# Optimization experiments

Hardware: AMD Instinct MI355X
Metric: run time of the kernel (lower is better)

Reference implementation:

```python
import jax, jax.numpy as jnp
import numpy as np

N = 50000      # nodes per graph type
E = 600000     # directed edges
F = 64         # raw node feature length
H = 128        # hidden / embedding size (embedding == h, so no padding needed)
STEPS = 4
G = 64         # graphs in batch


def setup_inputs() -> dict:
    key = jax.random.key(0)
    ks = jax.random.split(key, 16)
    s = 1.0 / np.sqrt(H)
    inp = {
        "atom_x": jax.random.normal(ks[0], (N, F), jnp.float32),
        "voro_x": jax.random.normal(ks[1], (N, F), jnp.float32),
        "atom_edge_index": jax.random.randint(ks[2], (2, E), 0, N, jnp.int64),
        "voro_edge_index": jax.random.randint(ks[3], (2, E), 0, N, jnp.int64),
        "batch": jnp.sort(jax.random.randint(ks[4], (N,), 0, G, jnp.int64)),
        # input embeddings (bias=False)
        "W_atom_in": jax.random.normal(ks[5], (F, H), jnp.float32) / np.sqrt(F),
        "W_voro_in": jax.random.normal(ks[6], (F, H), jnp.float32) / np.sqrt(F),
        # GatedGraphConv per-step message weights [STEPS, H, H]
        "atom_W": jax.random.normal(ks[7], (STEPS, H, H), jnp.float32) * s,
        "voro_W": jax.random.normal(ks[8], (STEPS, H, H), jnp.float32) * s,
        # GRUCell params (torch layout: W_ih [3H, H], gates ordered r, z, n)
        "atom_Wih": jax.random.normal(ks[9], (3 * H, H), jnp.float32) * s,
        "atom_Whh": jax.random.normal(ks[10], (3 * H, H), jnp.float32) * s,
        "atom_bih": jnp.zeros((3 * H,), jnp.float32),
        "atom_bhh": jnp.zeros((3 * H,), jnp.float32),
        "voro_Wih": jax.random.normal(ks[11], (3 * H, H), jnp.float32) * s,
        "voro_Whh": jax.random.normal(ks[12], (3 * H, H), jnp.float32) * s,
        "voro_bih": jnp.zeros((3 * H,), jnp.float32),
        "voro_bhh": jnp.zeros((3 * H,), jnp.float32),
        # prediction head Linear(2H, 1)
        "pred_W": jax.random.normal(ks[13], (2 * H, 1), jnp.float32) * s,
        "pred_b": jnp.zeros((1,), jnp.float32),
    }
    return inp


def _gated_graph_conv(x, edge_index, W, Wih, Whh, bih, bhh):
    """PyG GatedGraphConv with aggr='add': per step, m = h @ W_l, scatter-add
    messages from source to target, then GRUCell(m, h)."""
    src, dst = edge_index[0], edge_index[1]

    def step(h, Wl):
        m = h @ Wl                                           # [N, H]
        agg = jax.ops.segment_sum(m[src], dst, num_segments=N)  # gather+scatter-add
        gi = agg @ Wih.T + bih                               # input gates
        gh = h @ Whh.T + bhh                                 # hidden gates
        ir, iz, inn = jnp.split(gi, 3, axis=-1)
        hr, hz, hn = jnp.split(gh, 3, axis=-1)
        r = jax.nn.sigmoid(ir + hr)
        z = jax.nn.sigmoid(iz + hz)
        n = jnp.tanh(inn + r * hn)
        h_new = (1.0 - z) * n + z * h
        return h_new, None

    h, _ = jax.lax.scan(step, x, W)
    return h


def _mean_pool(x, batch):
    s = jax.ops.segment_sum(x, batch, num_segments=G)
    cnt = jax.ops.segment_sum(jnp.ones((x.shape[0],), x.dtype), batch, num_segments=G)
    return s / jnp.maximum(cnt, 1.0)[:, None]


def reference(atom_x, voro_x, atom_edge_index, voro_edge_index, batch,
              W_atom_in, W_voro_in, atom_W, voro_W,
              atom_Wih, atom_Whh, atom_bih, atom_bhh,
              voro_Wih, voro_Whh, voro_bih, voro_bhh,
              pred_W, pred_b):
    a = jnp.tanh(atom_x @ W_atom_in)                         # [N, H]
    v = jnp.tanh(voro_x @ W_voro_in)                         # [N, H]
    a = _gated_graph_conv(a, atom_edge_index, atom_W, atom_Wih, atom_Whh, atom_bih, atom_bhh)
    v = _gated_graph_conv(v, voro_edge_index, voro_W, voro_Wih, voro_Whh, voro_bih, voro_bhh)
    a = jax.nn.relu(_mean_pool(a, batch))                    # [G, H]
    v = jax.nn.relu(_mean_pool(v, batch))                    # [G, H]
    g = jnp.concatenate([a, v], axis=1)                      # [G, 2H]
    return (g @ pred_W + pred_b)[:, 0]                       # [G]
```

## Files before the change

kernel.cpp:

```cpp
#include <hip/hip_runtime.h>
#include <hip/hip_fp16.h>
#include <math.h>

#define HDIM 128
typedef unsigned short u16;
typedef __attribute__((ext_vector_type(8))) short bf16x8;
typedef __attribute__((ext_vector_type(4))) float f32x4;

__device__ __forceinline__ u16 f2bf(float x) {
    unsigned u = __float_as_uint(x);
    u = (u + 0x7FFFu + ((u >> 16) & 1u)) >> 16;
    return (u16)u;
}
__device__ __forceinline__ float bf2f(u16 h) {
    return __uint_as_float(((unsigned)h) << 16);
}
__device__ __forceinline__ bf16x8 ld8(const u16* p) {
    return *reinterpret_cast<const bf16x8*>(p);
}
__device__ __forceinline__ void split8(const float* v, bf16x8& hi, bf16x8& lo) {
#pragma unroll
    for (int j = 0; j < 8; ++j) {
        unsigned u = __float_as_uint(v[j]);
        unsigned h = (u + 0x7FFFu + ((u >> 16) & 1u)) >> 16;
        float rem = v[j] - __uint_as_float(h << 16);
        hi[j] = (short)h;
        lo[j] = (short)(__float_as_uint(rem) >> 16);
    }
}
__device__ __forceinline__ float2 up2(unsigned u) {
    __half2 h = *reinterpret_cast<__half2*>(&u);
    float2 f; f.x = __low2float(h); f.y = __high2float(h); return f;
}
__device__ __forceinline__ u16 f2h(float x) {
    __half t = __float2half(x);
    return *reinterpret_cast<u16*>(&t);
}
#define MFMA(acc, a, b) acc = __builtin_amdgcn_mfma_f32_16x16x32_bf16(a, b, acc, 0, 0, 0)

__global__ __launch_bounds__(256) void prep_wfull(const float* __restrict__ Ws,
                                                  const float* __restrict__ Wih,
                                                  u16* __restrict__ hi, u16* __restrict__ lo) {
    int s = blockIdx.y;
    int idx = blockIdx.x * 256 + threadIdx.x;
    int c2 = idx >> 7, r = idx & 127;
    const float* wr = Ws + (size_t)s * 16384 + (size_t)r * 128;
    const float* wc = Wih + (size_t)c2 * 128;
    float acc = 0.f;
#pragma unroll 8
    for (int k = 0; k < 128; k += 4) {
        float4 a = *reinterpret_cast<const float4*>(wr + k);
        float4 b = *reinterpret_cast<const float4*>(wc + k);
        acc += a.x * b.x + a.y * b.y + a.z * b.z + a.w * b.w;
    }
    size_t o = (size_t)s * 49152 + idx;
    u16 h = f2bf(acc);
    hi[o] = h; lo[o] = f2bf(acc - bf2f(h));
}

__global__ __launch_bounds__(256) void prep_split(const float* __restrict__ W,
                                                  u16* __restrict__ hi, u16* __restrict__ lo, int n) {
    int i = blockIdx.x * 256 + threadIdx.x;
    if (i < n) { float v = W[i]; u16 h = f2bf(v); hi[i] = h; lo[i] = f2bf(v - bf2f(h)); }
}

__global__ __launch_bounds__(256) void prep_win(const float* __restrict__ W,
                                                u16* __restrict__ hi, u16* __restrict__ lo) {
    int idx = blockIdx.x * 256 + threadIdx.x;
    int r = idx >> 6, c = idx & 63;
    float v = W[(size_t)c * 128 + r];
    u16 h = f2bf(v);
    hi[idx] = h; lo[idx] = f2bf(v - bf2f(h));
}

__global__ __launch_bounds__(256) void split_x2(const float* __restrict__ x0, const float* __restrict__ x1,
                                                u16* __restrict__ hi0, u16* __restrict__ lo0,
                                                u16* __restrict__ hi1, u16* __restrict__ lo1,
                                                int n, int ntot) {
    int i = blockIdx.x * 256 + threadIdx.x;
    if (i >= ntot) return;
    const float* x = blockIdx.y ? x1 : x0;
    u16* hi = blockIdx.y ? hi1 : hi0;
    u16* lo = blockIdx.y ? lo1 : lo0;
    float v = (i < n) ? x[i] : 0.f;
    u16 h = f2bf(v);
    hi[i] = h; lo[i] = f2bf(v - bf2f(h));
}

__global__ __launch_bounds__(256) void embed_k(const u16* __restrict__ Xhi0, const u16* __restrict__ Xlo0,
                                               const u16* __restrict__ Xhi1, const u16* __restrict__ Xlo1,
                                               const u16* __restrict__ Bhi0, const u16* __restrict__ Blo0,
                                               const u16* __restrict__ Bhi1, const u16* __restrict__ Blo1,
                                               float* __restrict__ Hf0, float* __restrict__ Hf1,
                                               u16* __restrict__ Hh0, u16* __restrict__ Hh1) {
    const int by = blockIdx.y;
    const u16* Xhi = by ? Xhi1 : Xhi0;  const u16* Xlo = by ? Xlo1 : Xlo0;
    const u16* Bhi = by ? Bhi1 : Bhi0;  const u16* Blo = by ? Blo1 : Blo0;
    float* Hf = by ? Hf1 : Hf0;
    u16* Hh = by ? Hh1 : Hh0;
    const int tid = threadIdx.x, wave = tid >> 6, lane = tid & 63;
    const int row0 = blockIdx.x * 32, cs = wave * 32;
    const int lr = lane & 15, lk = (lane >> 4) * 8;
    f32x4 acc[2][2];
#pragma unroll
    for (int i = 0; i < 2; ++i)
#pragma unroll
        for (int j = 0; j < 2; ++j) acc[i][j] = (f32x4)0.f;
#pragma unroll
    for (int kc = 0; kc < 2; ++kc) {
        const size_t ao = (size_t)(row0 + lr) * 64 + kc * 32 + lk;
        bf16x8 ah0 = ld8(Xhi + ao), ah1 = ld8(Xhi + ao + 16 * 64);
        bf16x8 al0 = ld8(Xlo + ao), al1 = ld8(Xlo + ao + 16 * 64);
#pragma unroll
        for (int cf = 0; cf < 2; ++cf) {
            const size_t bo = (size_t)(cs + cf * 16 + lr) * 64 + kc * 32 + lk;
            bf16x8 bh = ld8(Bhi + bo), bl = ld8(Blo + bo);
            MFMA(acc[0][cf], ah0, bh); MFMA(acc[0][cf], ah0, bl); MFMA(acc[0][cf], al0, bh);
            MFMA(acc[1][cf], ah1, bh); MFMA(acc[1][cf], ah1, bl); MFMA(acc[1][cf], al1, bh);
        }
    }
#pragma unroll
    for (int rf = 0; rf < 2; ++rf)
#pragma unroll
        for (int cf = 0; cf < 2; ++cf)
#pragma unroll
            for (int rg = 0; rg < 4; ++rg) {
                int row = row0 + rf * 16 + (lane >> 4) * 4 + rg;
                int col = cs + cf * 16 + lr;
                float v = tanhf(acc[rf][cf][rg]);
                size_t o = (size_t)row * HDIM + col;
                Hf[o] = v;
                Hh[o] = f2h(v);
            }
}

__global__ __launch_bounds__(512, 4) void step_k(const float* __restrict__ Hf0, const float* __restrict__ Hf1,
                                                 const u16* __restrict__ Hh0, const u16* __restrict__ Hh1,
                                                 const int* __restrict__ ro0, const int* __restrict__ ro1,
                                                 const int* __restrict__ ss0, const int* __restrict__ ss1,
                                                 const u16* __restrict__ Wf0h, const u16* __restrict__ Wf0l,
                                                 const u16* __restrict__ Wf1h, const u16* __restrict__ Wf1l,
                                                 const u16* __restrict__ Wh0h, const u16* __restrict__ Wh0l,
                                                 const u16* __restrict__ Wh1h, const u16* __restrict__ Wh1l,
                                                 const float* __restrict__ bi0, const float* __restrict__ bh0,
                                                 const float* __restrict__ bi1, const float* __restrict__ bh1,
                                                 float* __restrict__ Hn0, float* __restrict__ Hn1,
                                                 u16* __restrict__ Hnh0, u16* __restrict__ Hnh1, int Nn) {
    __shared__ u16 agh[32][136];
    __shared__ u16 agl[32][136];
    __shared__ u16 hhh[32][136];
    __shared__ u16 hhl[32][136];
    __shared__ int eidx[1024];
    const int by = blockIdx.y;
    const float* Hf = by ? Hf1 : Hf0;
    const u16* Hh = by ? Hh1 : Hh0;
    const int* row_off = by ? ro1 : ro0;
    const int* ssrc = by ? ss1 : ss0;
    const int tid = threadIdx.x, wave = tid >> 6, lane = tid & 63;
    const int row0 = blockIdx.x * 32;

    const int rowEnd = (row0 + 32 < Nn) ? row0 + 32 : Nn;
    const int eLo = row_off[row0];
    const int nE = row_off[rowEnd] - eLo;
    for (int i = tid; i < nE && i < 1024; i += 512) eidx[i] = ssrc[eLo + i];
    __syncthreads();

#pragma unroll
    for (int q = 0; q < 4; ++q) {
        const int nl = wave * 4 + q;
        const int node = row0 + nl;
        float ax = 0.f, ay = 0.f;
        if (node < Nn) {
            int lo = row_off[node] - eLo, hi = row_off[node + 1] - eLo;
            int hiS = (hi < 1024) ? hi : 1024;
            int i = lo;
            for (; i + 12 <= hiS; i += 12) {
                unsigned u[12];
#pragma unroll
                for (int j = 0; j < 12; ++j)
                    u[j] = *reinterpret_cast<const unsigned*>(Hh + (size_t)eidx[i + j] * HDIM + lane * 2);
#pragma unroll
                for (int j = 0; j < 12; ++j) { float2 v = up2(u[j]); ax += v.x; ay += v.y; }
            }
            for (; i + 4 <= hiS; i += 4) {
                unsigned u[4];
#pragma unroll
                for (int j = 0; j < 4; ++j)
                    u[j] = *reinterpret_cast<const unsigned*>(Hh + (size_t)eidx[i + j] * HDIM + lane * 2);
#pragma unroll
                for (int j = 0; j < 4; ++j) { float2 v = up2(u[j]); ax += v.x; ay += v.y; }
            }
            for (; i < hiS; ++i) {
                float2 v = up2(*reinterpret_cast<const unsigned*>(Hh + (size_t)eidx[i] * HDIM + lane * 2));
                ax += v.x; ay += v.y;
            }
            for (; i < hi; ++i) {
                float2 v = up2(*reinterpret_cast<const unsigned*>(Hh + (size_t)ssrc[eLo + i] * HDIM + lane * 2));
                ax += v.x; ay += v.y;
            }
        }
        u16 hx = f2bf(ax), hy = f2bf(ay);
        u16 lx = f2bf(ax - bf2f(hx)), ly = f2bf(ay - bf2f(hy));
        *reinterpret_cast<unsigned*>(&agh[nl][lane * 2]) = (unsigned)hx | ((unsigned)hy << 16);
        *reinterpret_cast<unsigned*>(&agl[nl][lane * 2]) = (unsigned)lx | ((unsigned)ly << 16);
    }

    {
        const int r = tid >> 4, c0 = (tid & 15) * 8;
        float v[8];
        const float* hp = Hf + (size_t)(row0 + r) * HDIM + c0;
        *reinterpret_cast<float4*>(&v[0]) = *reinterpret_cast<const float4*>(hp);
        *reinterpret_cast<float4*>(&v[4]) = *reinterpret_cast<const float4*>(hp + 4);
        bf16x8 hi, lo;
        split8(v, hi, lo);
        *reinterpret_cast<bf16x8*>(&hhh[r][c0]) = hi;
        *reinterpret_cast<bf16x8*>(&hhl[r][c0]) = lo;
    }
    __syncthreads();

    const u16* Wfhi = by ? Wf1h : Wf0h;  const u16* Wflo = by ? Wf1l : Wf0l;
    const u16* Whhi = by ? Wh1h : Wh0h;  const u16* Whlo = by ? Wh1l : Wh0l;
    const float* bih = by ? bi1 : bi0;   const float* bhh = by ? bh1 : bh0;
    float* Hnf = by ? Hn1 : Hn0;
    u16* Hnh = by ? Hnh1 : Hnh0;
    const int lr = lane & 15, lk = (lane >> 4) * 8, cs = wave * 16;
    f32x4 accI[2][3], accH[2][3];
#pragma unroll
    for (int rf = 0; rf < 2; ++rf)
#pragma unroll
        for (int g = 0; g < 3; ++g) { accI[rf][g] = (f32x4)0.f; accH[rf][g] = (f32x4)0.f; }
#pragma unroll
    for (int kc = 0; kc < 4; ++kc) {
        bf16x8 ga[2], gl[2], ha[2], hl[2];
#pragma unroll
        for (int rf = 0; rf < 2; ++rf) {
            const int rr = rf * 16 + lr, cc = kc * 32 + lk;
            ga[rf] = *reinterpret_cast<const bf16x8*>(&agh[rr][cc]);
            gl[rf] = *reinterpret_cast<const bf16x8*>(&agl[rr][cc]);
            ha[rf] = *reinterpret_cast<const bf16x8*>(&hhh[rr][cc]);
            hl[rf] = *reinterpret_cast<const bf16x8*>(&hhl[rr][cc]);
        }
#pragma unroll
        for (int g = 0; g < 3; ++g) {
            const size_t bo = (size_t)(g * 128 + cs + lr) * HDIM + kc * 32 + lk;
            bf16x8 fh = ld8(Wfhi + bo), fl = ld8(Wflo + bo);
            bf16x8 wh = ld8(Whhi + bo), wl = ld8(Whlo + bo);
#pragma unroll
            for (int rf = 0; rf < 2; ++rf) {
                MFMA(accI[rf][g], ga[rf], fh); MFMA(accI[rf][g], ga[rf], fl); MFMA(accI[rf][g], gl[rf], fh);
                MFMA(accH[rf][g], ha[rf], wh); MFMA(accH[rf][g], ha[rf], wl); MFMA(accH[rf][g], hl[rf], wh);
            }
        }
    }
    const int c = cs + lr;
    const float bir = bih[c], biz = bih[128 + c], bin = bih[256 + c];
    const float bhr = bhh[c], bhz = bhh[128 + c], bhn = bhh[256 + c];
#pragma unroll
    for (int rf = 0; rf < 2; ++rf)
#pragma unroll
        for (int rg = 0; rg < 4; ++rg) {
            const int rl = rf * 16 + (lane >> 4) * 4 + rg;
            const int row = row0 + rl;
            float gir = accI[rf][0][rg] + bir;
            float giz = accI[rf][1][rg] + biz;
            float gin = accI[rf][2][rg] + bin;
            float ghr = accH[rf][0][rg] + bhr;
            float ghz = accH[rf][1][rg] + bhz;
            float ghn = accH[rf][2][rg] + bhn;
            float r = 1.f / (1.f + expf(-(gir + ghr)));
            float z = 1.f / (1.f + expf(-(giz + ghz)));
            float nn = tanhf(gin + r * ghn);
            float hold = bf2f(hhh[rl][c]) + bf2f(hhl[rl][c]);
            float hn = (1.f - z) * nn + z * hold;
            size_t o = (size_t)row * HDIM + c;
            Hnf[o] = hn;
            Hnh[o] = f2h(hn);
        }
}

__global__ void zero_int2(int* p0, int* p1, int n) {
    int i = blockIdx.x * 256 + threadIdx.x;
    int* p = blockIdx.y ? p1 : p0;
    if (i < n) p[i] = 0;
}

__global__ void hist_k2(const int* __restrict__ d0, const int* __restrict__ d1,
                        int* __restrict__ c0, int* __restrict__ c1, int E) {
    int e = blockIdx.x * 256 + threadIdx.x;
    const int* dst = blockIdx.y ? d1 : d0;
    int* cnt = blockIdx.y ? c1 : c0;
    if (e < E) atomicAdd(&cnt[dst[e]], 1);
}

__global__ __launch_bounds__(1024) void scan_k2(int* __restrict__ c0, int* __restrict__ r0,
                                                int* __restrict__ c1, int* __restrict__ r1, int n) {
    int* cnt_cursor = blockIdx.x ? c1 : c0;
    int* row_off = blockIdx.x ? r1 : r0;
    __shared__ int wsum[16];
    __shared__ int carry_s;
    const int tid = threadIdx.x, lane = tid & 63, wv = tid >> 6;
    if (tid == 0) carry_s = 0;
    __syncthreads();
    for (int base = 0; base < n; base += 1024) {
        int i = base + tid;
        int v = (i < n) ? cnt_cursor[i] : 0;
        int x = v;
#pragma unroll
        for (int off = 1; off < 64; off <<= 1) {
            int t = __shfl_up(x, off);
            if (lane >= off) x += t;
        }
        if (lane == 63) wsum[wv] = x;
        __syncthreads();
        if (wv == 0 && lane < 16) {
            int s = wsum[lane];
#pragma unroll
            for (int off = 1; off < 16; off <<= 1) {
                int t = __shfl_up(s, off);
                if (lane >= off) s += t;
            }
            wsum[lane] = s;
        }
        __syncthreads();
        int wbase = (wv == 0) ? 0 : wsum[wv - 1];
        int carry = carry_s;
        int total = wsum[15];
        int excl = carry + wbase + x - v;
        if (i < n) { row_off[i] = excl; cnt_cursor[i] = excl; }
        __syncthreads();
        if (tid == 0) carry_s = carry + total;
        __syncthreads();
    }
    if (tid == 0) row_off[n] = carry_s;
}

__global__ void scatter_k2(const int* __restrict__ s0, const int* __restrict__ d0,
                           const int* __restrict__ s1, const int* __restrict__ d1,
                           int* __restrict__ c0, int* __restrict__ c1,
                           int* __restrict__ o0, int* __restrict__ o1, int E) {
    int e = blockIdx.x * 256 + threadIdx.x;
    const int* src = blockIdx.y ? s1 : s0;
    const int* dst = blockIdx.y ? d1 : d0;
    int* cursor = blockIdx.y ? c1 : c0;
    int* ssrc = blockIdx.y ? o1 : o0;
    if (e < E) {
        int p = atomicAdd(&cursor[dst[e]], 1);
        ssrc[p] = src[e];
    }
}

__global__ __launch_bounds__(256) void pool_k(const float* __restrict__ H0, const float* __restrict__ H1,
                                              const int* __restrict__ batch,
                                              float* __restrict__ p0, float* __restrict__ p1, int M) {
    const float* Hf = blockIdx.y ? H1 : H0;
    float* pooled = blockIdx.y ? p1 : p0;
    __shared__ int lo_s, hi_s;
    __shared__ float smx[256], smy[256];
    int g = blockIdx.x;
    if (threadIdx.x == 0) {
        int lo = 0, hi = M;
        while (lo < hi) { int mid = (lo + hi) >> 1; if (batch[mid] < g) lo = mid + 1; else hi = mid; }
        lo_s = lo;
        int lo2 = lo, hi2 = M;
        while (lo2 < hi2) { int mid = (lo2 + hi2) >> 1; if (batch[mid] < g + 1) lo2 = mid + 1; else hi2 = mid; }
        hi_s = lo2;
    }
    __syncthreads();
    int lo = lo_s, hi = hi_s;
    int c2 = threadIdx.x & 63, quarter = threadIdx.x >> 6;
    float ax = 0.f, ay = 0.f;
    for (int i = lo + quarter; i < hi; i += 4) {
        float2 v = *reinterpret_cast<const float2*>(Hf + (size_t)i * HDIM + c2 * 2);
        ax += v.x; ay += v.y;
    }
    smx[threadIdx.x] = ax; smy[threadIdx.x] = ay;
    __syncthreads();
    if (quarter == 0) {
        float sx = smx[c2] + smx[c2 + 64] + smx[c2 + 128] + smx[c2 + 192];
        float sy = smy[c2] + smy[c2 + 64] + smy[c2 + 128] + smy[c2 + 192];
        float cnt = (float)(hi - lo); if (cnt < 1.f) cnt = 1.f;
        pooled[g * HDIM + c2 * 2]     = fmaxf(sx / cnt, 0.f);
        pooled[g * HDIM + c2 * 2 + 1] = fmaxf(sy / cnt, 0.f);
    }
}

__global__ void pred_kernel(const float* __restrict__ pa, const float* __restrict__ pv,
                            const float* __restrict__ pW, const float* __restrict__ pb,
                            float* __restrict__ out) {
    int g = blockIdx.x, lane = threadIdx.x;
    float s = pa[g * HDIM + lane] * pW[lane]
            + pa[g * HDIM + 64 + lane] * pW[64 + lane]
            + pv[g * HDIM + lane] * pW[HDIM + lane]
            + pv[g * HDIM + 64 + lane] * pW[192 + lane];
    for (int off = 32; off; off >>= 1) s += __shfl_down(s, off);
    if (lane == 0) out[g] = s + pb[0];
}

extern "C" void kernel_launch(void* const* d_in, const int* in_sizes, int n_in,
                              void* d_out, int out_size, void* d_ws, size_t ws_size,
                              hipStream_t stream) {
    const float* atom_x   = (const float*)d_in[0];
    const float* voro_x   = (const float*)d_in[1];
    const int*   atom_ei  = (const int*)d_in[2];
    const int*   voro_ei  = (const int*)d_in[3];
    const int*   batch    = (const int*)d_in[4];
    const float* W_at_in  = (const float*)d_in[5];
    const float* W_vo_in  = (const float*)d_in[6];
    const float* atom_W   = (const float*)d_in[7];
    const float* voro_W   = (const float*)d_in[8];
    const float* atom_Wih = (const float*)d_in[9];
    const float* atom_Whh = (const float*)d_in[10];
    const float* atom_bih = (const float*)d_in[11];
    const float* atom_bhh = (const float*)d_in[12];
    const float* voro_Wih = (const float*)d_in[13];
    const float* voro_Whh = (const float*)d_in[14];
    const float* voro_bih = (const float*)d_in[15];
    const float* voro_bhh = (const float*)d_in[16];
    const float* pred_W   = (const float*)d_in[17];
    const float* pred_b   = (const float*)d_in[18];
    float* out = (float*)d_out;

    const int Nn = in_sizes[4];
    const int Ee = in_sizes[2] / 2;
    const int Gg = out_size;
    const int Npad = (Nn + 31) & ~31;

    char* base = (char*)d_ws;
    size_t off = 0;
    auto alloc = [&](size_t bytes) -> char* {
        char* p = base + off;
        off = (off + bytes + 255) & ~(size_t)255;
        return p;
    };

    float *Hf[2], *Hnf[2];
    u16 *HhA[2], *HhB[2];
    u16 *Xhi[2], *Xlo[2];
    u16 *WfHi[2], *WfLo[2], *WhHi[2], *WhLo[2], *WnHi[2], *WnLo[2];
    int *row_off[2], *cursor[2], *ssrc[2];
    for (int t = 0; t < 2; ++t) {
        Hf[t]  = (float*)alloc((size_t)Npad * HDIM * 4);
        Hnf[t] = (float*)alloc((size_t)Npad * HDIM * 4);
        HhA[t] = (u16*)alloc((size_t)Npad * HDIM * 2);
        HhB[t] = (u16*)alloc((size_t)Npad * HDIM * 2);
        Xhi[t] = (u16*)Hnf[t];
        Xlo[t] = Xhi[t] + (size_t)Npad * 64;
        WfHi[t] = (u16*)alloc(4 * 49152 * 2); WfLo[t] = (u16*)alloc(4 * 49152 * 2);
        WhHi[t] = (u16*)alloc(384 * 128 * 2); WhLo[t] = (u16*)alloc(384 * 128 * 2);
        WnHi[t] = (u16*)alloc(128 * 64 * 2);  WnLo[t] = (u16*)alloc(128 * 64 * 2);
        row_off[t] = (int*)alloc((size_t)(Nn + 1) * 4);
        cursor[t]  = (int*)alloc((size_t)Nn * 4);
        ssrc[t]    = (int*)alloc((size_t)Ee * 4);
    }
    float* pooledA = (float*)alloc((size_t)Gg * HDIM * 4);
    float* pooledV = (float*)alloc((size_t)Gg * HDIM * 4);

    const float* Wst[2] = {atom_W, voro_W};
    const float* Wih[2] = {atom_Wih, voro_Wih};
    const float* Whh[2] = {atom_Whh, voro_Whh};
    const float* Win[2] = {W_at_in, W_vo_in};

    for (int t = 0; t < 2; ++t) {
        prep_wfull<<<dim3(192, 4), 256, 0, stream>>>(Wst[t], Wih[t], WfHi[t], WfLo[t]);
        prep_split<<<192, 256, 0, stream>>>(Whh[t], WhHi[t], WhLo[t], 384 * 128);
        prep_win<<<32, 256, 0, stream>>>(Win[t], WnHi[t], WnLo[t]);
    }

    const int eb  = (Ee + 255) / 256;
    const int nb  = (Nn + 255) / 256;
    const int gbs = Npad / 32;

    split_x2<<<dim3((Npad * 64 + 255) / 256, 2), 256, 0, stream>>>(
        atom_x, voro_x, Xhi[0], Xlo[0], Xhi[1], Xlo[1], Nn * 64, Npad * 64);
    embed_k<<<dim3(gbs, 2), 256, 0, stream>>>(Xhi[0], Xlo[0], Xhi[1], Xlo[1],
                                              WnHi[0], WnLo[0], WnHi[1], WnLo[1],
                                              Hf[0], Hf[1], HhA[0], HhA[1]);

    zero_int2<<<dim3(nb, 2), 256, 0, stream>>>(cursor[0], cursor[1], Nn);
    hist_k2<<<dim3(eb, 2), 256, 0, stream>>>(atom_ei + Ee, voro_ei + Ee, cursor[0], cursor[1], Ee);
    scan_k2<<<2, 1024, 0, stream>>>(cursor[0], row_off[0], cursor[1], row_off[1], Nn);
    scatter_k2<<<dim3(eb, 2), 256, 0, stream>>>(atom_ei, atom_ei + Ee, voro_ei, voro_ei + Ee,
                                                cursor[0], cursor[1], ssrc[0], ssrc[1], Ee);

    float *hA0 = Hf[0], *hB0 = Hnf[0], *hA1 = Hf[1], *hB1 = Hnf[1];
    u16 *gA0 = HhA[0], *gB0 = HhB[0], *gA1 = HhA[1], *gB1 = HhB[1];
    for (int s = 0; s < 4; ++s) {
        step_k<<<dim3(gbs, 2), 512, 0, stream>>>(
            hA0, hA1, gA0, gA1, row_off[0], row_off[1], ssrc[0], ssrc[1],
            WfHi[0] + (size_t)s * 49152, WfLo[0] + (size_t)s * 49152,
            WfHi[1] + (size_t)s * 49152, WfLo[1] + (size_t)s * 49152,
            WhHi[0], WhLo[0], WhHi[1], WhLo[1],
            atom_bih, atom_bhh, voro_bih, voro_bhh,
            hB0, hB1, gB0, gB1, Nn);
        float* tp;
        tp = hA0; hA0 = hB0; hB0 = tp;
        tp = hA1; hA1 = hB1; hB1 = tp;
        u16* up;
        up = gA0; gA0 = gB0; gB0 = up;
        up = gA1; gA1 = gB1; gB1 = up;
    }
    pool_k<<<dim3(Gg, 2), 256, 0, stream>>>(hA0, hA1, batch, pooledA, pooledV, Nn);
    pred_kernel<<<Gg, 64, 0, stream>>>(pooledA, pooledV, pred_W, pred_b, out);
}
```

Baseline: 1.166 ms.

## Drop fp32 hidden-state copy and interleave gathers across four nodes per wave

Removes the fp32 copy of the hidden state. Embedding, step and pooling kernels now read and write only the 16-bit copy, which cuts global traffic and workspace, and the input split buffers alias the spare 16-bit buffer. The neighbour aggregation now handles a wave's four nodes together, issuing 16 masked gathers per iteration up to the largest degree to raise memory-level parallelism. The cost is lower precision on the carried hidden state and wasted loads when degrees are imbalanced.

```diff
diff --git a/kernel.cpp b/kernel.cpp
--- a/kernel.cpp
+++ b/kernel.cpp
@@ -91,12 +91,10 @@
                                                const u16* __restrict__ Xhi1, const u16* __restrict__ Xlo1,
                                                const u16* __restrict__ Bhi0, const u16* __restrict__ Blo0,
                                                const u16* __restrict__ Bhi1, const u16* __restrict__ Blo1,
-                                               float* __restrict__ Hf0, float* __restrict__ Hf1,
                                                u16* __restrict__ Hh0, u16* __restrict__ Hh1) {
     const int by = blockIdx.y;
     const u16* Xhi = by ? Xhi1 : Xhi0;  const u16* Xlo = by ? Xlo1 : Xlo0;
     const u16* Bhi = by ? Bhi1 : Bhi0;  const u16* Blo = by ? Blo1 : Blo0;
-    float* Hf = by ? Hf1 : Hf0;
     u16* Hh = by ? Hh1 : Hh0;
     const int tid = threadIdx.x, wave = tid >> 6, lane = tid & 63;
     const int row0 = blockIdx.x * 32, cs = wave * 32;
@@ -127,15 +125,11 @@
             for (int rg = 0; rg < 4; ++rg) {
                 int row = row0 + rf * 16 + (lane >> 4) * 4 + rg;
                 int col = cs + cf * 16 + lr;
-                float v = tanhf(acc[rf][cf][rg]);
-                size_t o = (size_t)row * HDIM + col;
-                Hf[o] = v;
-                Hh[o] = f2h(v);
+                Hh[(size_t)row * HDIM + col] = f2h(tanhf(acc[rf][cf][rg]));
             }
 }
 
-__global__ __launch_bounds__(512, 4) void step_k(const float* __restrict__ Hf0, const float* __restrict__ Hf1,
-                                                 const u16* __restrict__ Hh0, const u16* __restrict__ Hh1,
+__global__ __launch_bounds__(512, 4) void step_k(const u16* __restrict__ Hh0, const u16* __restrict__ Hh1,
                                                  const int* __restrict__ ro0, const int* __restrict__ ro1,
                                                  const int* __restrict__ ss0, const int* __restrict__ ss1,
                                                  const u16* __restrict__ Wf0h, const u16* __restrict__ Wf0l,
@@ -144,15 +138,13 @@
                                                  const u16* __restrict__ Wh1h, const u16* __restrict__ Wh1l,
                                                  const float* __restrict__ bi0, const float* __restrict__ bh0,
                                                  const float* __restrict__ bi1, const float* __restrict__ bh1,
-                                                 float* __restrict__ Hn0, float* __restrict__ Hn1,
-                                                 u16* __restrict__ Hnh0, u16* __restrict__ Hnh1, int Nn) {
+                                                 u16* __restrict__ Hn0, u16* __restrict__ Hn1, int Nn) {
     __shared__ u16 agh[32][136];
     __shared__ u16 agl[32][136];
     __shared__ u16 hhh[32][136];
     __shared__ u16 hhl[32][136];
     __shared__ int eidx[1024];
     const int by = blockIdx.y;
-    const float* Hf = by ? Hf1 : Hf0;
     const u16* Hh = by ? Hh1 : Hh0;
     const int* row_off = by ? ro1 : ro0;
     const int* ssrc = by ? ss1 : ss0;
@@ -165,52 +157,74 @@
     for (int i = tid; i < nE && i < 1024; i += 512) eidx[i] = ssrc[eLo + i];
     __syncthreads();
 
-#pragma unroll
-    for (int q = 0; q < 4; ++q) {
-        const int nl = wave * 4 + q;
-        const int node = row0 + nl;
-        float ax = 0.f, ay = 0.f;
-        if (node < Nn) {
-            int lo = row_off[node] - eLo, hi = row_off[node + 1] - eLo;
-            int hiS = (hi < 1024) ? hi : 1024;
-            int i = lo;
-            for (; i + 12 <= hiS; i += 12) {
-                unsigned u[12];
-#pragma unroll
-                for (int j = 0; j < 12; ++j)
-                    u[j] = *reinterpret_cast<const unsigned*>(Hh + (size_t)eidx[i + j] * HDIM + lane * 2);
-#pragma unroll
-                for (int j = 0; j < 12; ++j) { float2 v = up2(u[j]); ax += v.x; ay += v.y; }
+    {
+        int lo4[4], hi4[4];
+        int mdeg = 0;
+#pragma unroll
+        for (int q = 0; q < 4; ++q) {
+            const int node = row0 + wave * 4 + q;
+            if (node < Nn) {
+                lo4[q] = __builtin_amdgcn_readfirstlane(row_off[node]) - eLo;
+                hi4[q] = __builtin_amdgcn_readfirstlane(row_off[node + 1]) - eLo;
+            } else { lo4[q] = 0; hi4[q] = 0; }
+            int d = hi4[q] - lo4[q];
+            mdeg = (d > mdeg) ? d : mdeg;
+        }
+        const int maxIter = (mdeg + 3) >> 2;
+        float ax[4], ay[4];
+#pragma unroll
+        for (int q = 0; q < 4; ++q) { ax[q] = 0.f; ay[q] = 0.f; }
+        for (int it = 0; it < maxIter; ++it) {
+            unsigned uu[16];
+            float ww[16];
+#pragma unroll
+            for (int q = 0; q < 4; ++q) {
+                const int base = lo4[q] + it * 4;
+#pragma unroll
+                for (int j = 0; j < 4; ++j) {
+                    const int p = base + j;
+                    const bool val = p < hi4[q];
+                    const int ps = val ? p : 0;
+                    int idx = (ps < 1024) ? eidx[ps] : ssrc[eLo + ps];
+                    idx = val ? idx : 0;
+                    uu[q * 4 + j] = *reinterpret_cast<const unsigned*>(Hh + (size_t)idx * HDIM + lane * 2);
+                    ww[q * 4 + j] = val ? 1.f : 0.f;
+                }
             }
-            for (; i + 4 <= hiS; i += 4) {
-                unsigned u[4];
-#pragma unroll
-                for (int j = 0; j < 4; ++j)
-                    u[j] = *reinterpret_cast<const unsigned*>(Hh + (size_t)eidx[i + j] * HDIM + lane * 2);
-#pragma unroll
-                for (int j = 0; j < 4; ++j) { float2 v = up2(u[j]); ax += v.x; ay += v.y; }
-            }
-            for (; i < hiS; ++i) {
-                float2 v = up2(*reinterpret_cast<const unsigned*>(Hh + (size_t)eidx[i] * HDIM + lane * 2));
-                ax += v.x; ay += v.y;
-            }
-            for (; i < hi; ++i) {
-                float2 v = up2(*reinterpret_cast<const unsigned*>(Hh + (size_t)ssrc[eLo + i] * HDIM + lane * 2));
-                ax += v.x; ay += v.y;
-            }
-        }
-        u16 hx = f2bf(ax), hy = f2bf(ay);
-        u16 lx = f2bf(ax - bf2f(hx)), ly = f2bf(ay - bf2f(hy));
-        *reinterpret_cast<unsigned*>(&agh[nl][lane * 2]) = (unsigned)hx | ((unsigned)hy << 16);
-        *reinterpret_cast<unsigned*>(&agl[nl][lane * 2]) = (unsigned)lx | ((unsigned)ly << 16);
+#pragma unroll
+            for (int q = 0; q < 4; ++q)
+#pragma unroll
+                for (int j = 0; j < 4; ++j) {
+                    float2 v = up2(uu[q * 4 + j]);
+                    ax[q] = fmaf(ww[q * 4 + j], v.x, ax[q]);
+                    ay[q] = fmaf(ww[q * 4 + j], v.y, ay[q]);
+                }
+        }
+#pragma unroll
+        for (int q = 0; q < 4; ++q) {
+            const int nl = wave * 4 + q;
+            u16 hx = f2bf(ax[q]), hy = f2bf(ay[q]);
+            u16 lx = f2bf(ax[q] - bf2f(hx)), ly = f2bf(ay[q] - bf2f(hy));
+            *reinterpret_cast<unsigned*>(&agh[nl][lane * 2]) = (unsigned)hx | ((unsigned)hy << 16);
+            *reinterpret_cast<unsigned*>(&agl[nl][lane * 2]) = (unsigned)lx | ((unsigned)ly << 16);
+        }
     }
 
     {
         const int r = tid >> 4, c0 = (tid & 15) * 8;
         float v[8];
-        const float* hp = Hf + (size_t)(row0 + r) * HDIM + c0;
-        *reinterpret_cast<float4*>(&v[0]) = *reinterpret_cast<const float4*>(hp);
-        *reinterpret_cast<float4*>(&v[4]) = *reinterpret_cast<const float4*>(hp + 4);
+        const int row = row0 + r;
+        if (row < Nn) {
+            const u16* hp = Hh + (size_t)row * HDIM + c0;
+#pragma unroll
+            for (int j = 0; j < 4; ++j) {
+                float2 f = up2(*reinterpret_cast<const unsigned*>(hp + j * 2));
+                v[j * 2] = f.x; v[j * 2 + 1] = f.y;
+            }
+        } else {
+#pragma unroll
+            for (int j = 0; j < 8; ++j) v[j] = 0.f;
+        }
         bf16x8 hi, lo;
         split8(v, hi, lo);
         *reinterpret_cast<bf16x8*>(&hhh[r][c0]) = hi;
@@ -221,8 +235,7 @@
     const u16* Wfhi = by ? Wf1h : Wf0h;  const u16* Wflo = by ? Wf1l : Wf0l;
     const u16* Whhi = by ? Wh1h : Wh0h;  const u16* Whlo = by ? Wh1l : Wh0l;
     const float* bih = by ? bi1 : bi0;   const float* bhh = by ? bh1 : bh0;
-    float* Hnf = by ? Hn1 : Hn0;
-    u16* Hnh = by ? Hnh1 : Hnh0;
+    u16* Hnh = by ? Hn1 : Hn0;
     const int lr = lane & 15, lk = (lane >> 4) * 8, cs = wave * 16;
     f32x4 accI[2][3], accH[2][3];
 #pragma unroll
@@ -272,9 +285,7 @@
             float nn = tanhf(gin + r * ghn);
             float hold = bf2f(hhh[rl][c]) + bf2f(hhl[rl][c]);
             float hn = (1.f - z) * nn + z * hold;
-            size_t o = (size_t)row * HDIM + c;
-            Hnf[o] = hn;
-            Hnh[o] = f2h(hn);
+            if (row < Nn) Hnh[(size_t)row * HDIM + c] = f2h(hn);
         }
 }
 
@@ -349,10 +360,10 @@
     }
 }
 
-__global__ __launch_bounds__(256) void pool_k(const float* __restrict__ H0, const float* __restrict__ H1,
+__global__ __launch_bounds__(256) void pool_k(const u16* __restrict__ H0, const u16* __restrict__ H1,
                                               const int* __restrict__ batch,
                                               float* __restrict__ p0, float* __restrict__ p1, int M) {
-    const float* Hf = blockIdx.y ? H1 : H0;
+    const u16* Hf = blockIdx.y ? H1 : H0;
     float* pooled = blockIdx.y ? p1 : p0;
     __shared__ int lo_s, hi_s;
     __shared__ float smx[256], smy[256];
@@ -370,7 +381,7 @@
     int c2 = threadIdx.x & 63, quarter = threadIdx.x >> 6;
     float ax = 0.f, ay = 0.f;
     for (int i = lo + quarter; i < hi; i += 4) {
-        float2 v = *reinterpret_cast<const float2*>(Hf + (size_t)i * HDIM + c2 * 2);
+        float2 v = up2(*reinterpret_cast<const unsigned*>(Hf + (size_t)i * HDIM + c2 * 2));
         ax += v.x; ay += v.y;
     }
     smx[threadIdx.x] = ax; smy[threadIdx.x] = ay;
@@ -433,18 +444,15 @@
         return p;
     };
 
-    float *Hf[2], *Hnf[2];
     u16 *HhA[2], *HhB[2];
     u16 *Xhi[2], *Xlo[2];
     u16 *WfHi[2], *WfLo[2], *WhHi[2], *WhLo[2], *WnHi[2], *WnLo[2];
     int *row_off[2], *cursor[2], *ssrc[2];
     for (int t = 0; t < 2; ++t) {
-        Hf[t]  = (float*)alloc((size_t)Npad * HDIM * 4);
-        Hnf[t] = (float*)alloc((size_t)Npad * HDIM * 4);
         HhA[t] = (u16*)alloc((size_t)Npad * HDIM * 2);
         HhB[t] = (u16*)alloc((size_t)Npad * HDIM * 2);
-        Xhi[t] = (u16*)Hnf[t];
-        Xlo[t] = Xhi[t] + (size_t)Npad * 64;
+        Xhi[t] = HhB[t];
+        Xlo[t] = HhB[t] + (size_t)Npad * 64;
         WfHi[t] = (u16*)alloc(4 * 49152 * 2); WfLo[t] = (u16*)alloc(4 * 49152 * 2);
         WhHi[t] = (u16*)alloc(384 * 128 * 2); WhLo[t] = (u16*)alloc(384 * 128 * 2);
         WnHi[t] = (u16*)alloc(128 * 64 * 2);  WnLo[t] = (u16*)alloc(128 * 64 * 2);
@@ -474,7 +482,7 @@
         atom_x, voro_x, Xhi[0], Xlo[0], Xhi[1], Xlo[1], Nn * 64, Npad * 64);
     embed_k<<<dim3(gbs, 2), 256, 0, stream>>>(Xhi[0], Xlo[0], Xhi[1], Xlo[1],
                                               WnHi[0], WnLo[0], WnHi[1], WnLo[1],
-                                              Hf[0], Hf[1], HhA[0], HhA[1]);
+                                              HhA[0], HhA[1]);
 
     zero_int2<<<dim3(nb, 2), 256, 0, stream>>>(cursor[0], cursor[1], Nn);
     hist_k2<<<dim3(eb, 2), 256, 0, stream>>>(atom_ei + Ee, voro_ei + Ee, cursor[0], cursor[1], Ee);
@@ -482,23 +490,19 @@
     scatter_k2<<<dim3(eb, 2), 256, 0, stream>>>(atom_ei, atom_ei + Ee, voro_ei, voro_ei + Ee,
                                                 cursor[0], cursor[1], ssrc[0], ssrc[1], Ee);
 
-    float *hA0 = Hf[0], *hB0 = Hnf[0], *hA1 = Hf[1], *hB1 = Hnf[1];
     u16 *gA0 = HhA[0], *gB0 = HhB[0], *gA1 = HhA[1], *gB1 = HhB[1];
     for (int s = 0; s < 4; ++s) {
         step_k<<<dim3(gbs, 2), 512, 0, stream>>>(
-            hA0, hA1, gA0, gA1, row_off[0], row_off[1], ssrc[0], ssrc[1],
+            gA0, gA1, row_off[0], row_off[1], ssrc[0], ssrc[1],
             WfHi[0] + (size_t)s * 49152, WfLo[0] + (size_t)s * 49152,
             WfHi[1] + (size_t)s * 49152, WfLo[1] + (size_t)s * 49152,
             WhHi[0], WhLo[0], WhHi[1], WhLo[1],
             atom_bih, atom_bhh, voro_bih, voro_bhh,
-            hB0, hB1, gB0, gB1, Nn);
-        float* tp;
-        tp = hA0; hA0 = hB0; hB0 = tp;
-        tp = hA1; hA1 = hB1; hB1 = tp;
+            gB0, gB1, Nn);
         u16* up;
         up = gA0; gA0 = gB0; gB0 = up;
         up = gA1; gA1 = gB1; gB1 = up;
     }
-    pool_k<<<dim3(Gg, 2), 256, 0, stream>>>(hA0, hA1, batch, pooledA, pooledV, Nn);
+    pool_k<<<dim3(Gg, 2), 256, 0, stream>>>(gA0, gA1, batch, pooledA, pooledV, Nn);
     pred_kernel<<<Gg, 64, 0, stream>>>(pooledA, pooledV, pred_W, pred_b, out);
 }
```

New measurement: 1.541 ms. 1.32x slower.
